# Kernel tuning notes

Measured on AMD Instinct MI355X. Metric: run time of the kernel, lower is better.

## Reference

```python
import jax, jax.numpy as jnp
import numpy as np

N = 50000      # num nodes
E = 800000     # num directed edges (before self loops)
C_IN = 128     # input channels
HID = 128      # hidden channels per head
H = 2          # attention heads (layer 0)
NEG_SLOPE = 0.2


def setup_inputs() -> dict:
    key = jax.random.key(0)
    ks = jax.random.split(key, 10)
    s = 0.05
    return {
        "x": jax.random.normal(ks[0], (N, C_IN), jnp.float32),
        "edge_index": jax.random.randint(ks[1], (2, E), 0, N, dtype=jnp.int32),
        "W1": jax.random.normal(ks[2], (C_IN, H * HID), jnp.float32) * s,
        "att_src1": jax.random.normal(ks[3], (H, HID), jnp.float32) * s,
        "att_dst1": jax.random.normal(ks[4], (H, HID), jnp.float32) * s,
        "b1": jax.random.normal(ks[5], (H * HID,), jnp.float32) * s,
        "W2": jax.random.normal(ks[6], (H * HID, 1), jnp.float32) * s,
        "att_src2": jax.random.normal(ks[7], (1, 1), jnp.float32) * s,
        "att_dst2": jax.random.normal(ks[8], (1, 1), jnp.float32) * s,
        "b2": jax.random.normal(ks[9], (1,), jnp.float32) * s,
    }


def gat_layer(x, src, dst, W, att_src, att_dst, bias, heads, out_ch, concat, num_nodes):
    # linear projection -> [N, H, C]
    h = (x @ W).reshape(num_nodes, heads, out_ch)
    a_src = jnp.einsum("nhc,hc->nh", h, att_src)  # [N, H]
    a_dst = jnp.einsum("nhc,hc->nh", h, att_dst)  # [N, H]
    # edge attention logits, LeakyReLU as in GATConv
    alpha = jax.nn.leaky_relu(a_src[src] + a_dst[dst], NEG_SLOPE)  # [Etot, H]
    # segment softmax over incoming edges of each destination node
    amax = jax.ops.segment_max(alpha, dst, num_segments=num_nodes)
    amax = jnp.where(jnp.isfinite(amax), amax, 0.0)
    ex = jnp.exp(alpha - amax[dst])
    denom = jax.ops.segment_sum(ex, dst, num_segments=num_nodes)
    coef = ex / (denom[dst] + 1e-16)                      # [Etot, H]
    # weighted scatter-aggregate of source features
    msg = h[src] * coef[:, :, None]                       # [Etot, H, C]
    out = jax.ops.segment_sum(msg, dst, num_segments=num_nodes)  # [N, H, C]
    out = out.reshape(num_nodes, heads * out_ch) if concat else out.mean(axis=1)
    return out + bias


def reference(x, edge_index, W1, att_src1, att_dst1, b1, W2, att_src2, att_dst2, b2):
    n = x.shape[0]
    loops = jnp.arange(n, dtype=edge_index.dtype)
    src = jnp.concatenate([edge_index[0], loops])  # GATConv adds self-loops
    dst = jnp.concatenate([edge_index[1], loops])
    h = gat_layer(x, src, dst, W1, att_src1, att_dst1, b1, H, HID, True, n)
    h = jax.nn.relu(h)
    out = gat_layer(h, src, dst, W2, att_src2, att_dst2, b2, 1, 1, False, n)
    return jax.nn.sigmoid(out)  # [N, 1]
```

## Files before the change

### kernel.cpp

```cpp
#include <hip/hip_runtime.h>
#include <hip/hip_bf16.h>

#define NEG_SLOPE 0.2f
#define MAXDEG 64

using f16x8 = __attribute__((ext_vector_type(8))) _Float16;
using f32x4 = __attribute__((ext_vector_type(4))) float;

__device__ inline unsigned short f2bf(float f) {
  __hip_bfloat16 b = __float2bfloat16(f);
  return __builtin_bit_cast(unsigned short, b);
}
__device__ inline unsigned short f2h(float f) {
  return __builtin_bit_cast(unsigned short, (_Float16)f);
}
__device__ inline float h2f(unsigned short u) {
  return (float)__builtin_bit_cast(_Float16, u);
}

__global__ __launch_bounds__(256) void k_pre(
    const float* __restrict__ W1, _Float16* __restrict__ W1T,
    int* __restrict__ cnt, int N) {
  const int b = blockIdx.x, t = threadIdx.x;
  if (b < 128) {
    const int e = b * 256 + t;
    const int k = e >> 8, c = e & 255;
    W1T[c * 128 + k] = (_Float16)W1[e];
  } else {
    const int i = (b - 128) * 256 + t;
    if (i < N) cnt[i] = 0;
  }
}

__global__ __launch_bounds__(256) void k_fused(
    const float* __restrict__ x, const _Float16* __restrict__ W1T,
    const float* __restrict__ att_src, const float* __restrict__ att_dst,
    _Float16* __restrict__ h1f, float4* __restrict__ attn, int N,
    const int* __restrict__ ei, int E, int Etot,
    int* __restrict__ cnt, int* __restrict__ rec) {
  __shared__ _Float16 xs[64][136];
  const int nGemm = (N + 63) >> 6;
  const int b = blockIdx.x;
  const int t = threadIdx.x;

  if (b >= nGemm) {
    const int e = (b - nGemm) * 256 + t;
    if (e < Etot) {
      int s, d;
      if (e < E) { s = ei[e]; d = ei[E + e]; } else { s = e - E; d = s; }
      const int slot = atomicAdd(&cnt[d], 1);
      if (slot < MAXDEG) rec[d * MAXDEG + slot] = s;
    }
    return;
  }

  const int w = t >> 6, l = t & 63;
  const int n0 = b * 64;
  {
    const int col4 = (t & 31) * 4;
#pragma unroll
    for (int p = 0; p < 8; ++p) {
      const int row = p * 8 + (t >> 5);
      float4 xv = make_float4(0.f, 0.f, 0.f, 0.f);
      if (n0 + row < N) xv = *(const float4*)(x + (size_t)(n0 + row) * 128 + col4);
      ushort4 u;
      u.x = f2h(xv.x); u.y = f2h(xv.y); u.z = f2h(xv.z); u.w = f2h(xv.w);
      *(ushort4*)&xs[row][col4] = u;
    }
  }
  __syncthreads();

  f32x4 acc[16];
#pragma unroll
  for (int nf = 0; nf < 16; ++nf) acc[nf] = f32x4{0.f, 0.f, 0.f, 0.f};
  const int cb = l & 15;
  const int kof = (l >> 4) * 8;
  const int xr = w * 16 + cb;
#pragma unroll
  for (int kk = 0; kk < 4; ++kk) {
    const f16x8 bx = *(const f16x8*)&xs[xr][kk * 32 + kof];
#pragma unroll
    for (int nf = 0; nf < 16; ++nf) {
      const f16x8 aw = *(const f16x8*)(W1T + (size_t)(nf * 16 + cb) * 128 + kk * 32 + kof);
      acc[nf] = __builtin_amdgcn_mfma_f32_16x16x32_f16(aw, bx, acc[nf], 0, 0, 0);
    }
  }

  const int node = n0 + w * 16 + cb;
  const int cg = (l >> 4) * 4;
  if (node < N) {
#pragma unroll
    for (int nf = 0; nf < 16; ++nf) {
      ushort4 u;
      u.x = f2h(acc[nf][0]); u.y = f2h(acc[nf][1]);
      u.z = f2h(acc[nf][2]); u.w = f2h(acc[nf][3]);
      *(ushort4*)(h1f + (size_t)node * 256 + nf * 16 + cg) = u;
    }
  }

  float s0 = 0.f, s1 = 0.f, d0 = 0.f, d1 = 0.f;
#pragma unroll
  for (int nf = 0; nf < 16; ++nf) {
    const float4 av = *(const float4*)(att_src + nf * 16 + cg);
    const float4 dv = *(const float4*)(att_dst + nf * 16 + cg);
    const float ls = acc[nf][0] * av.x + acc[nf][1] * av.y + acc[nf][2] * av.z + acc[nf][3] * av.w;
    const float ld = acc[nf][0] * dv.x + acc[nf][1] * dv.y + acc[nf][2] * dv.z + acc[nf][3] * dv.w;
    if (nf < 8) { s0 += ls; d0 += ld; } else { s1 += ls; d1 += ld; }
  }
  s0 += __shfl_xor(s0, 16); s0 += __shfl_xor(s0, 32);
  s1 += __shfl_xor(s1, 16); s1 += __shfl_xor(s1, 32);
  d0 += __shfl_xor(d0, 16); d0 += __shfl_xor(d0, 32);
  d1 += __shfl_xor(d1, 16); d1 += __shfl_xor(d1, 32);
  if (l < 16 && node < N) attn[node] = make_float4(s0, s1, d0, d1);
}

__global__ __launch_bounds__(256) void k3_gather(
    const int* __restrict__ cnt, const int* __restrict__ rec,
    const float4* __restrict__ attn, const _Float16* __restrict__ h1f,
    const float* __restrict__ b1, const float* __restrict__ W2,
    float* __restrict__ h2, int N) {
  const int wave = threadIdx.x >> 6, lane = threadIdx.x & 63;
  const int n = blockIdx.x * 4 + wave;
  if (n >= N) return;
  const bool hi = lane >= 32;
  const int deg = cnt[n];
  const int kcnt = deg < MAXDEG ? deg : MAXDEG;
  float4 acc = {0.f, 0.f, 0.f, 0.f};
  float den = 0.f;
  const unsigned short* h1u = (const unsigned short*)h1f;
  const float4 an = attn[n];

  int sv = 0, wp = 0;
  if (lane < kcnt) {
    sv = rec[n * MAXDEG + lane];
    const float4 a4 = attn[sv];
    float a0 = a4.x + an.z;
    float a1 = a4.y + an.w;
    a0 = a0 > 0.f ? a0 : a0 * NEG_SLOPE;
    a1 = a1 > 0.f ? a1 : a1 * NEG_SLOPE;
    wp = (int)(((unsigned)f2bf(__expf(a1)) << 16) | f2bf(__expf(a0)));
  }

  int s0_ = __shfl(sv, 0), s1_ = __shfl(sv, 1), s2_ = __shfl(sv, 2), s3_ = __shfl(sv, 3);
  ushort4 h0 = ((const ushort4*)(h1u + (size_t)s0_ * 256))[lane];
  ushort4 h1 = ((const ushort4*)(h1u + (size_t)s1_ * 256))[lane];
  ushort4 h2v = ((const ushort4*)(h1u + (size_t)s2_ * 256))[lane];
  ushort4 h3 = ((const ushort4*)(h1u + (size_t)s3_ * 256))[lane];

  for (int i = 0; i < kcnt; i += 4) {
    const int j0 = (i + 4) & 63, j1 = (i + 5) & 63, j2 = (i + 6) & 63, j3 = (i + 7) & 63;
    const int t0 = __shfl(sv, j0), t1 = __shfl(sv, j1), t2 = __shfl(sv, j2), t3 = __shfl(sv, j3);
    const ushort4 g0 = ((const ushort4*)(h1u + (size_t)t0 * 256))[lane];
    const ushort4 g1 = ((const ushort4*)(h1u + (size_t)t1 * 256))[lane];
    const ushort4 g2 = ((const ushort4*)(h1u + (size_t)t2 * 256))[lane];
    const ushort4 g3 = ((const ushort4*)(h1u + (size_t)t3 * 256))[lane];

    const unsigned int wp0 = (unsigned)__shfl(wp, i);
    const unsigned int wp1 = (unsigned)__shfl(wp, i + 1);
    const unsigned int wp2 = (unsigned)__shfl(wp, i + 2);
    const unsigned int wp3 = (unsigned)__shfl(wp, i + 3);
    const float w0 = __uint_as_float(hi ? (wp0 & 0xffff0000u) : (wp0 << 16));
    const float w1 = __uint_as_float(hi ? (wp1 & 0xffff0000u) : (wp1 << 16));
    const float w2 = __uint_as_float(hi ? (wp2 & 0xffff0000u) : (wp2 << 16));
    const float w3 = __uint_as_float(hi ? (wp3 & 0xffff0000u) : (wp3 << 16));

    acc.x = fmaf(h2f(h0.x), w0, acc.x); acc.y = fmaf(h2f(h0.y), w0, acc.y);
    acc.z = fmaf(h2f(h0.z), w0, acc.z); acc.w = fmaf(h2f(h0.w), w0, acc.w);
    acc.x = fmaf(h2f(h1.x), w1, acc.x); acc.y = fmaf(h2f(h1.y), w1, acc.y);
    acc.z = fmaf(h2f(h1.z), w1, acc.z); acc.w = fmaf(h2f(h1.w), w1, acc.w);
    acc.x = fmaf(h2f(h2v.x), w2, acc.x); acc.y = fmaf(h2f(h2v.y), w2, acc.y);
    acc.z = fmaf(h2f(h2v.z), w2, acc.z); acc.w = fmaf(h2f(h2v.w), w2, acc.w);
    acc.x = fmaf(h2f(h3.x), w3, acc.x); acc.y = fmaf(h2f(h3.y), w3, acc.y);
    acc.z = fmaf(h2f(h3.z), w3, acc.z); acc.w = fmaf(h2f(h3.w), w3, acc.w);
    den += w0 + w1 + w2 + w3;

    h0 = g0; h1 = g1; h2v = g2; h3 = g3;
  }

  const float inv = 1.f / (den + 1e-16f);
  const float4 bv = ((const float4*)b1)[lane];
  const float4 wv4 = ((const float4*)W2)[lane];
  float p = 0.f;
  p += fmaxf(fmaf(acc.x, inv, bv.x), 0.f) * wv4.x;
  p += fmaxf(fmaf(acc.y, inv, bv.y), 0.f) * wv4.y;
  p += fmaxf(fmaf(acc.z, inv, bv.z), 0.f) * wv4.z;
  p += fmaxf(fmaf(acc.w, inv, bv.w), 0.f) * wv4.w;
  for (int m = 32; m; m >>= 1) p += __shfl_xor(p, m);
  if (lane == 0) h2[n] = p;
}

__global__ __launch_bounds__(256) void k_l2(
    const int* __restrict__ cnt, const int* __restrict__ rec,
    const float* __restrict__ h2,
    const float* __restrict__ att_s2, const float* __restrict__ att_d2,
    const float* __restrict__ b2, float* __restrict__ out, int N) {
  const int sub = threadIdx.x & 15;
  const int n = blockIdx.x * 16 + (threadIdx.x >> 4);
  if (n >= N) return;
  const float as2 = att_s2[0];
  const float hd = h2[n] * att_d2[0];
  const int m = min(cnt[n], MAXDEG);
  float num = 0.f, den = 0.f;
  for (int base = 0; base < m; base += 16) {
    if (base + sub < m) {
      const float hs = h2[rec[n * MAXDEG + base + sub]];
      float a = fmaf(hs, as2, hd);
      a = a > 0.f ? a : a * NEG_SLOPE;
      const float w = __expf(a);
      den += w;
      num = fmaf(w, hs, num);
    }
  }
  for (int mm = 8; mm; mm >>= 1) { num += __shfl_xor(num, mm); den += __shfl_xor(den, mm); }
  if (sub == 0) {
    const float v = num / (den + 1e-16f) + b2[0];
    out[n] = 1.f / (1.f + __expf(-v));
  }
}

extern "C" void kernel_launch(void* const* d_in, const int* in_sizes, int n_in,
                              void* d_out, int out_size, void* d_ws, size_t ws_size,
                              hipStream_t stream) {
  const float* x        = (const float*)d_in[0];
  const int*   ei       = (const int*)d_in[1];
  const float* W1       = (const float*)d_in[2];
  const float* att_src1 = (const float*)d_in[3];
  const float* att_dst1 = (const float*)d_in[4];
  const float* b1       = (const float*)d_in[5];
  const float* W2       = (const float*)d_in[6];
  const float* att_s2   = (const float*)d_in[7];
  const float* att_d2   = (const float*)d_in[8];
  const float* b2       = (const float*)d_in[9];
  float* out = (float*)d_out;

  const int N = in_sizes[0] / 128;
  const int E = in_sizes[1] / 2;
  const int Etot = E + N;

  char* ws = (char*)d_ws;
  size_t o = 0;
  float4* attn = (float4*)(ws + o); o += (size_t)N * 16;
  int* rec     = (int*)(ws + o); o += (size_t)N * MAXDEG * 4;
  _Float16* h1f = (_Float16*)(ws + o); o += (size_t)N * 256 * 2;
  _Float16* W1T = (_Float16*)(ws + o); o += (size_t)256 * 128 * 2;
  float* h2  = (float*)(ws + o); o += (size_t)N * 4;
  int* cnt   = (int*)(ws + o); o += (size_t)N * 4;

  const int nGemm = (N + 63) / 64;
  const int nScat = (Etot + 255) / 256;
  k_pre<<<128 + (N + 255) / 256, 256, 0, stream>>>(W1, W1T, cnt, N);
  k_fused<<<nGemm + nScat, 256, 0, stream>>>(x, W1T, att_src1, att_dst1,
                                             h1f, attn, N, ei, E, Etot, cnt, rec);
  k3_gather<<<(N + 3) / 4, 256, 0, stream>>>(cnt, rec, attn, h1f, b1, W2, h2, N);
  k_l2<<<(N + 15) / 16, 256, 0, stream>>>(cnt, rec, h2, att_s2, att_d2, b2, out, N);
}
```

Before: 224.7 us.

## Fold W1 transpose into fused GEMM via LDS staging and grid-stride edge scatter

Removes the separate pre-kernel. Each GEMM block now converts W1 to fp16 and transposes it into shared memory per K-chunk, and the count buffer is zeroed with a memset instead. The edge-scatter part moves to a fixed set of 1024 grid-stride blocks placed first in the grid, so scatter work is scheduled ahead of the GEMM tiles, and launch bounds request higher occupancy. The aim is to save one kernel launch and the W1T round trip. The cost is that every GEMM block re-reads and converts the full fp32 W1 with strided global loads, plus extra barriers per K-chunk.

Measured after the change: 233.8 us. 1.04x slower.

```diff
diff --git a/kernel.cpp b/kernel.cpp
--- a/kernel.cpp
+++ b/kernel.cpp
@@ -18,34 +18,18 @@
   return (float)__builtin_bit_cast(_Float16, u);
 }
 
-__global__ __launch_bounds__(256) void k_pre(
-    const float* __restrict__ W1, _Float16* __restrict__ W1T,
-    int* __restrict__ cnt, int N) {
-  const int b = blockIdx.x, t = threadIdx.x;
-  if (b < 128) {
-    const int e = b * 256 + t;
-    const int k = e >> 8, c = e & 255;
-    W1T[c * 128 + k] = (_Float16)W1[e];
-  } else {
-    const int i = (b - 128) * 256 + t;
-    if (i < N) cnt[i] = 0;
-  }
-}
-
-__global__ __launch_bounds__(256) void k_fused(
-    const float* __restrict__ x, const _Float16* __restrict__ W1T,
+__global__ __launch_bounds__(256, 4) void k_fused(
+    const float* __restrict__ x, const float* __restrict__ W1,
     const float* __restrict__ att_src, const float* __restrict__ att_dst,
     _Float16* __restrict__ h1f, float4* __restrict__ attn, int N,
     const int* __restrict__ ei, int E, int Etot,
-    int* __restrict__ cnt, int* __restrict__ rec) {
+    int* __restrict__ cnt, int* __restrict__ rec, int nScat) {
   __shared__ _Float16 xs[64][136];
-  const int nGemm = (N + 63) >> 6;
-  const int b = blockIdx.x;
-  const int t = threadIdx.x;
-
-  if (b >= nGemm) {
-    const int e = (b - nGemm) * 256 + t;
-    if (e < Etot) {
+  __shared__ _Float16 wT[256][40];
+  const int b = blockIdx.x, t = threadIdx.x;
+
+  if (b < nScat) {
+    for (int e = b * 256 + t; e < Etot; e += nScat * 256) {
       int s, d;
       if (e < E) { s = ei[e]; d = ei[E + e]; } else { s = e - E; d = s; }
       const int slot = atomicAdd(&cnt[d], 1);
@@ -55,7 +39,8 @@
   }
 
   const int w = t >> 6, l = t & 63;
-  const int n0 = b * 64;
+  const int tile = b - nScat;
+  const int n0 = tile * 64;
   {
     const int col4 = (t & 31) * 4;
 #pragma unroll
@@ -68,7 +53,6 @@
       *(ushort4*)&xs[row][col4] = u;
     }
   }
-  __syncthreads();
 
   f32x4 acc[16];
 #pragma unroll
@@ -76,33 +60,39 @@
   const int cb = l & 15;
   const int kof = (l >> 4) * 8;
   const int xr = w * 16 + cb;
-#pragma unroll
+
   for (int kk = 0; kk < 4; ++kk) {
+    __syncthreads();
+#pragma unroll 8
+    for (int k = 0; k < 32; ++k)
+      wT[t][k] = (_Float16)W1[(kk * 32 + k) * 256 + t];
+    __syncthreads();
+
     const f16x8 bx = *(const f16x8*)&xs[xr][kk * 32 + kof];
 #pragma unroll
     for (int nf = 0; nf < 16; ++nf) {
-      const f16x8 aw = *(const f16x8*)(W1T + (size_t)(nf * 16 + cb) * 128 + kk * 32 + kof);
+      const f16x8 aw = *(const f16x8*)&wT[nf * 16 + cb][kof];
       acc[nf] = __builtin_amdgcn_mfma_f32_16x16x32_f16(aw, bx, acc[nf], 0, 0, 0);
     }
   }
 
   const int node = n0 + w * 16 + cb;
-  const int cg = (l >> 4) * 4;
+  const int cg_ = (l >> 4) * 4;
   if (node < N) {
 #pragma unroll
     for (int nf = 0; nf < 16; ++nf) {
       ushort4 u;
       u.x = f2h(acc[nf][0]); u.y = f2h(acc[nf][1]);
       u.z = f2h(acc[nf][2]); u.w = f2h(acc[nf][3]);
-      *(ushort4*)(h1f + (size_t)node * 256 + nf * 16 + cg) = u;
+      *(ushort4*)(h1f + (size_t)node * 256 + nf * 16 + cg_) = u;
     }
   }
 
   float s0 = 0.f, s1 = 0.f, d0 = 0.f, d1 = 0.f;
 #pragma unroll
   for (int nf = 0; nf < 16; ++nf) {
-    const float4 av = *(const float4*)(att_src + nf * 16 + cg);
-    const float4 dv = *(const float4*)(att_dst + nf * 16 + cg);
+    const float4 av = *(const float4*)(att_src + nf * 16 + cg_);
+    const float4 dv = *(const float4*)(att_dst + nf * 16 + cg_);
     const float ls = acc[nf][0] * av.x + acc[nf][1] * av.y + acc[nf][2] * av.z + acc[nf][3] * av.w;
     const float ld = acc[nf][0] * dv.x + acc[nf][1] * dv.y + acc[nf][2] * dv.z + acc[nf][3] * dv.w;
     if (nf < 8) { s0 += ls; d0 += ld; } else { s1 += ls; d1 += ld; }
@@ -242,15 +232,16 @@
   float4* attn = (float4*)(ws + o); o += (size_t)N * 16;
   int* rec     = (int*)(ws + o); o += (size_t)N * MAXDEG * 4;
   _Float16* h1f = (_Float16*)(ws + o); o += (size_t)N * 256 * 2;
-  _Float16* W1T = (_Float16*)(ws + o); o += (size_t)256 * 128 * 2;
   float* h2  = (float*)(ws + o); o += (size_t)N * 4;
   int* cnt   = (int*)(ws + o); o += (size_t)N * 4;
 
+  hipMemsetAsync(cnt, 0, (size_t)N * 4, stream);
+
+  const int nScat = 1024;
   const int nGemm = (N + 63) / 64;
-  const int nScat = (Etot + 255) / 256;
-  k_pre<<<128 + (N + 255) / 256, 256, 0, stream>>>(W1, W1T, cnt, N);
-  k_fused<<<nGemm + nScat, 256, 0, stream>>>(x, W1T, att_src1, att_dst1,
-                                             h1f, attn, N, ei, E, Etot, cnt, rec);
+  k_fused<<<nScat + nGemm, 256, 0, stream>>>(x, W1, att_src1, att_dst1,
+                                             h1f, attn, N, ei, E, Etot,
+                                             cnt, rec, nScat);
   k3_gather<<<(N + 3) / 4, 256, 0, stream>>>(cnt, rec, attn, h1f, b1, W2, h2, N);
   k_l2<<<(N + 15) / 16, 256, 0, stream>>>(cnt, rec, h2, att_s2, att_d2, b2, out, N);
 }
```
